# Performance work log

Measured on AMD Instinct MI355X. Metric: run time of the kernel, lower is better.

The kernel has to match this reference:

```python
import jax, jax.numpy as jnp
import numpy as np

NUM_EXPERTS = 8
TOP_K = 2
HIDDEN = 768
FFN = 3072
B, S = 4, 4096


def setup_inputs() -> dict:
    key = jax.random.key(0)
    ks = jax.random.split(key, 7)
    scale_h = 1.0 / np.sqrt(HIDDEN)
    scale_f = 1.0 / np.sqrt(FFN)
    return {
        "hidden_states": jax.random.normal(ks[0], (B, S, HIDDEN), dtype=jnp.float32),
        "router_w": jax.random.normal(ks[1], (HIDDEN, NUM_EXPERTS), dtype=jnp.float32) * scale_h,
        "router_b": jnp.zeros((NUM_EXPERTS,), dtype=jnp.float32),
        "w1": jax.random.normal(ks[2], (NUM_EXPERTS, HIDDEN, FFN), dtype=jnp.float32) * scale_h,
        "b1": jnp.zeros((NUM_EXPERTS, FFN), dtype=jnp.float32),
        "w2": jax.random.normal(ks[3], (NUM_EXPERTS, FFN, HIDDEN), dtype=jnp.float32) * scale_f,
        "b2": jnp.zeros((NUM_EXPERTS, HIDDEN), dtype=jnp.float32),
    }


def _moe_forward(x_flat, router_w, router_b, w1, b1, w2, b2):
    T = x_flat.shape[0]
    # Router: logits [T, E]
    router_logits = x_flat @ router_w + router_b
    routing_weights = jax.nn.softmax(router_logits, axis=-1)
    # Top-k gating: softmax over the selected top-k logits
    top_vals, top_idx = jax.lax.top_k(router_logits, TOP_K)
    top_gates = jax.nn.softmax(top_vals, axis=-1)
    # Scatter gates into dense dispatch mask [T, E]
    rows = jnp.arange(T)[:, None]
    dispatch_mask = jnp.zeros_like(routing_weights).at[rows, top_idx].set(top_gates)
    # Expert computation: combined = sum_e gate[:, e] * FFN_e(x)
    # (tokens with zero gate contribute exactly 0, matching the torch scatter-combine)
    combined = jnp.zeros_like(x_flat)
    for e in range(NUM_EXPERTS):
        h = jax.nn.gelu(x_flat @ w1[e] + b1[e])  # [T, FFN]
        y = h @ w2[e] + b2[e]                    # [T, HIDDEN]
        combined = combined + dispatch_mask[:, e:e + 1] * y
    # Auxiliary load-balancing loss
    mean_routing_prob = jnp.mean(routing_weights, axis=0)
    tokens_per_expert = jnp.sum(dispatch_mask, axis=0) / T
    aux_loss = jnp.sum(mean_routing_prob * tokens_per_expert) * NUM_EXPERTS
    return combined, routing_weights, dispatch_mask, aux_loss, router_logits


def reference(hidden_states, router_w, router_b, w1, b1, w2, b2):
    batch, seq, hid = hidden_states.shape
    x_flat = hidden_states.reshape(-1, hid)
    combined, routing_weights, dispatch_mask, aux_loss, router_logits = _moe_forward(
        x_flat, router_w, router_b, w1, b1, w2, b2)
    E = NUM_EXPERTS
    return (
        combined.reshape(batch, seq, hid),            # expert_outputs
        routing_weights.reshape(batch, seq, E),       # routing_weights
        dispatch_mask.reshape(batch, seq, E),         # dispatch_mask
        aux_loss,                                     # aux_loss
        router_logits.reshape(batch, seq, E),         # router_logits
    )
```

## Files before the change

kernel.cpp:

```cpp
#include <hip/hip_runtime.h>
#include <math.h>

#define TOKENS 16384
#define HID 768
#define FFN_DIM 3072
#define NEXP 8
#define MAXT 136

#define RT_TPB 128
#define RT_BLOCKS (TOKENS / RT_TPB)

typedef __bf16 bf16x8 __attribute__((ext_vector_type(8)));
typedef float f32x4 __attribute__((ext_vector_type(4)));

#define GLOBAL_AS(p) ((const __attribute__((address_space(1))) void*)(p))
#define LDS_AS(p)    ((__attribute__((address_space(3))) void*)(p))

__device__ __forceinline__ float gelu_f(float x) {
    const float x3 = x * x * x;
    const float z = 0.7978845608028654f * (x + 0.044715f * x3);
    const float e = __expf(2.f * z);
    const float t = 1.f - 2.f / (e + 1.f);
    return 0.5f * x * (1.f + t);
}

__device__ __forceinline__ unsigned short f2bf(float v) {
    return __builtin_bit_cast(unsigned short, (__bf16)v);
}

__global__ void __launch_bounds__(512) router_kernel(
    const float* __restrict__ x, const float* __restrict__ rw,
    const float* __restrict__ rb,
    float* __restrict__ out_rw, float* __restrict__ out_dm,
    float* __restrict__ out_logits,
    int* __restrict__ counts, float* __restrict__ probsum,
    float* __restrict__ gatesum, int* __restrict__ lists,
    float* __restrict__ glists)
{
    __shared__ int s_cnt[NEXP], s_base[NEXP];
    __shared__ float s_prob[NEXP], s_gate[NEXP];
    __shared__ int s_e1[RT_TPB], s_s1[RT_TPB], s_e2[RT_TPB], s_s2[RT_TPB];
    __shared__ float s_g1v[RT_TPB], s_g2v[RT_TPB];

    const int tid = threadIdx.x;
    if (tid < NEXP) { s_cnt[tid] = 0; s_prob[tid] = 0.f; s_gate[tid] = 0.f; }
    __syncthreads();

    const int wave = tid >> 6, lane = tid & 63;

    for (int it = 0; it < RT_TPB / 8; ++it) {
        const int lt = wave * (RT_TPB / 8) + it;
        const int t = blockIdx.x * RT_TPB + lt;
        const float* xr = x + (size_t)t * HID;
        float acc[NEXP];
#pragma unroll
        for (int e = 0; e < NEXP; ++e) acc[e] = 0.f;
#pragma unroll
        for (int j = 0; j < 12; ++j) {
            const int i = lane + (j << 6);
            const float xv = xr[i];
            const float4 a = ((const float4*)(rw + (size_t)i * NEXP))[0];
            const float4 b = ((const float4*)(rw + (size_t)i * NEXP))[1];
            acc[0] += xv * a.x; acc[1] += xv * a.y; acc[2] += xv * a.z; acc[3] += xv * a.w;
            acc[4] += xv * b.x; acc[5] += xv * b.y; acc[6] += xv * b.z; acc[7] += xv * b.w;
        }
#pragma unroll
        for (int off = 32; off > 0; off >>= 1)
#pragma unroll
            for (int e = 0; e < NEXP; ++e) acc[e] += __shfl_down(acc[e], off, 64);

        if (lane == 0) {
            float lg[NEXP];
            float m = -1e30f;
#pragma unroll
            for (int e = 0; e < NEXP; ++e) { lg[e] = acc[e] + rb[e]; m = fmaxf(m, lg[e]); }
            float ex[NEXP]; float s = 0.f;
#pragma unroll
            for (int e = 0; e < NEXP; ++e) { ex[e] = expf(lg[e] - m); s += ex[e]; }
            const float inv = 1.f / s;
            float* lrow = out_logits + (size_t)t * NEXP;
            float* prow = out_rw + (size_t)t * NEXP;
#pragma unroll
            for (int e = 0; e < NEXP; ++e) {
                lrow[e] = lg[e];
                const float p = ex[e] * inv;
                prow[e] = p;
                atomicAdd(&s_prob[e], p);
            }
            int i1 = 0;
#pragma unroll
            for (int e = 1; e < NEXP; ++e) if (lg[e] > lg[i1]) i1 = e;
            int i2 = (i1 == 0) ? 1 : 0;
#pragma unroll
            for (int e = 0; e < NEXP; ++e) if (e != i1 && lg[e] > lg[i2]) i2 = e;
            const float e2 = expf(lg[i2] - lg[i1]);
            const float g1 = 1.f / (1.f + e2);
            const float g2 = e2 / (1.f + e2);
            out_dm[(size_t)t * NEXP + i1] = g1;
            out_dm[(size_t)t * NEXP + i2] = g2;
            atomicAdd(&s_gate[i1], g1);
            atomicAdd(&s_gate[i2], g2);
            s_e1[lt] = i1; s_s1[lt] = atomicAdd(&s_cnt[i1], 1); s_g1v[lt] = g1;
            s_e2[lt] = i2; s_s2[lt] = atomicAdd(&s_cnt[i2], 1); s_g2v[lt] = g2;
        }
    }
    __syncthreads();
    if (tid < NEXP) {
        s_base[tid] = atomicAdd(&counts[tid], s_cnt[tid]);
        atomicAdd(&probsum[tid], s_prob[tid]);
        atomicAdd(&gatesum[tid], s_gate[tid]);
    }
    __syncthreads();
    if (tid < RT_TPB) {
        const int t = blockIdx.x * RT_TPB + tid;
        int e = s_e1[tid]; int p = s_base[e] + s_s1[tid];
        lists[e * TOKENS + p] = t; glists[e * TOKENS + p] = s_g1v[tid];
        e = s_e2[tid]; p = s_base[e] + s_s2[tid];
        lists[e * TOKENS + p] = t; glists[e * TOKENS + p] = s_g2v[tid];
    }
}

__global__ void finalize_kernel(const int* __restrict__ counts,
                                const float* __restrict__ probsum,
                                const float* __restrict__ gatesum,
                                int* __restrict__ poffs,
                                float* __restrict__ out_aux)
{
    if (threadIdx.x == 0 && blockIdx.x == 0) {
        float s = 0.f; int po = 0;
        for (int e = 0; e < NEXP; ++e) {
            poffs[e] = po;
            po += ((counts[e] + 255) >> 8) << 8;
            s += (probsum[e] / (float)TOKENS) * (gatesum[e] / (float)TOKENS);
        }
        poffs[NEXP] = po;
        *out_aux = s * (float)NEXP;
    }
}

__global__ void __launch_bounds__(192) gatherx_kernel(
    const float* __restrict__ x, const int* __restrict__ counts,
    const int* __restrict__ poffs, const int* __restrict__ lists,
    unsigned short* __restrict__ Xg)
{
    const int r = blockIdx.x;
    if (r >= poffs[NEXP]) return;
    int e = 0;
#pragma unroll
    for (int q = 1; q < NEXP; ++q) e += (r >= poffs[q]);
    const int ri = r - poffs[e];
    const int tid = threadIdx.x;
    uint2 o = make_uint2(0u, 0u);
    if (ri < counts[e]) {
        const int tok = lists[e * TOKENS + ri];
        const float4 v = *(const float4*)&x[(size_t)tok * HID + tid * 4];
        o.x = (unsigned)f2bf(v.x) | ((unsigned)f2bf(v.y) << 16);
        o.y = (unsigned)f2bf(v.z) | ((unsigned)f2bf(v.w) << 16);
    }
    *(uint2*)&Xg[(size_t)r * HID + tid * 4] = o;
}

__global__ void __launch_bounds__(256) convT_kernel(const float* __restrict__ in,
                                                    unsigned short* __restrict__ out,
                                                    int R, int C)
{
    __shared__ float sT[32][65];
    const int e = blockIdx.z;
    const float* in_e = in + (size_t)e * R * C;
    unsigned short* out_e = out + (size_t)e * R * C;
    const int r0 = blockIdx.y * 64;
    const int c0 = blockIdx.x * 32;
    const int tid = threadIdx.x;
    const int rr = tid >> 3, c4 = (tid & 7) * 4;
#pragma unroll
    for (int half = 0; half < 2; ++half) {
        const int r = rr + half * 32;
        const float4 v = *(const float4*)&in_e[(size_t)(r0 + r) * C + c0 + c4];
        sT[c4 + 0][r] = v.x; sT[c4 + 1][r] = v.y;
        sT[c4 + 2][r] = v.z; sT[c4 + 3][r] = v.w;
    }
    __syncthreads();
    const int c = tid >> 3, u = tid & 7;
    uint4 pk;
    const float* sr = &sT[c][u * 8];
    pk.x = (unsigned)f2bf(sr[0]) | ((unsigned)f2bf(sr[1]) << 16);
    pk.y = (unsigned)f2bf(sr[2]) | ((unsigned)f2bf(sr[3]) << 16);
    pk.z = (unsigned)f2bf(sr[4]) | ((unsigned)f2bf(sr[5]) << 16);
    pk.w = (unsigned)f2bf(sr[6]) | ((unsigned)f2bf(sr[7]) << 16);
    *(uint4*)&out_e[(size_t)(c0 + c) * R + r0 + u * 8] = pk;
}


#define STAGE1(bufE_, kt_) do { \
    _Pragma("unroll") \
    for (int _kh = 0; _kh < 2; ++_kh) { \
        const unsigned short* _pa = aStP + (kt_) * 64 + _kh * 32; \
        const unsigned short* _pb = bStP + (kt_) * 64 + _kh * 32; \
        __builtin_amdgcn_global_load_lds(GLOBAL_AS(_pa),           LDS_AS(aD + (bufE_) + _kh * 4096),       16, 0, 0); \
        __builtin_amdgcn_global_load_lds(GLOBAL_AS(_pa + 16 * KS), LDS_AS(aD + (bufE_) + _kh * 4096 + 512), 16, 0, 0); \
        __builtin_amdgcn_global_load_lds(GLOBAL_AS(_pb),           LDS_AS(bD + (bufE_) + _kh * 4096),       16, 0, 0); \
        __builtin_amdgcn_global_load_lds(GLOBAL_AS(_pb + 16 * KS), LDS_AS(bD + (bufE_) + _kh * 4096 + 512), 16, 0, 0); \
    } \
} while (0)

#define COMPUTE_TILE(curE_) do { \
    _Pragma("unroll") \
    for (int kh = 0; kh < 2; ++kh) { \
        bf16x8 af[4], bb[4]; \
        _Pragma("unroll") \
        for (int t = 0; t < 4; ++t) { \
            af[t] = *(const bf16x8*)&lds[(curE_) + kh * 4096 + (wm + t * 16 + fr) * 32 + swzR]; \
            bb[t] = *(const bf16x8*)&lds[16384 + (curE_) + kh * 4096 + (wn + t * 16 + fr) * 32 + swzR]; \
        } \
        _Pragma("unroll") \
        for (int tm = 0; tm < 4; ++tm) \
            _Pragma("unroll") \
            for (int tn = 0; tn < 4; ++tn) \
                acc[tm][tn] = __builtin_amdgcn_mfma_f32_16x16x32_bf16( \
                    af[tm], bb[tn], acc[tm][tn], 0, 0, 0); \
    } \
} while (0)

#define DECODE_TILE(NT_, MT_) \
    const int nwg = gridDim.x;                                                       \
    const int orig = blockIdx.x;                                                     \
    const int qq = nwg >> 3, rr2 = nwg & 7;                                          \
    const int xcd = orig & 7, pos = orig >> 3;                                       \
    const int wid = (xcd < rr2 ? xcd * (qq + 1) : rr2 * (qq + 1) + (xcd - rr2) * qq) + pos; \
    const int nSuper = (MT_) >> 3;                                                   \
    const int fullB = nSuper * 8 * (NT_);                                            \
    int mt, nti;                                                                     \
    if (wid < fullB) {                                                               \
        const int st_ = wid / (8 * (NT_));                                           \
        const int lo = wid - st_ * (8 * (NT_));                                      \
        mt = (st_ << 3) + (lo & 7);                                                  \
        nti = lo >> 3;                                                               \
    } else {                                                                         \
        const int rem = (MT_) - (nSuper << 3);                                       \
        const int lo = wid - fullB;                                                  \
        mt = (nSuper << 3) + lo % rem;                                               \
        nti = lo / rem;                                                              \
    }

__global__ void __launch_bounds__(256, 2) gemm1_kernel(
    const unsigned short* __restrict__ Xg, const unsigned short* __restrict__ W1T,
    const float* __restrict__ b1, const int* __restrict__ poffs,
    unsigned short* __restrict__ H, int grBase, int mtCount)
{
    extern __shared__ __bf16 lds[];
    const int KS = HID;
    const int NKT = HID / 64;

    DECODE_TILE(FFN_DIM / 128, mtCount)
    const int gr = grBase + mt * 128;
    if (gr >= poffs[NEXP]) return;
    int e = 0;
#pragma unroll
    for (int q = 1; q < NEXP; ++q) e += (gr >= poffs[q]);
    const int hbase = gr - grBase;
    const int n0 = nti * 128;

    const int tid = threadIdx.x;
    const int wv = tid >> 6, lane = tid & 63;
    const int wm = (wv >> 1) * 64, wn = (wv & 1) * 64;
    const int fr = lane & 15, q4 = lane >> 4;
    const int rowoff = lane >> 2;
    const int swzW = ((lane & 3) ^ ((lane >> 3) & 3)) << 3;
    const int swzR = (q4 ^ ((fr >> 1) & 3)) << 3;

    const unsigned short* aStP = Xg + (size_t)(gr + wv * 32 + rowoff) * KS + swzW;
    const unsigned short* bStP = W1T + (size_t)e * (HID * FFN_DIM)
                               + (size_t)(n0 + wv * 32 + rowoff) * KS + swzW;
    __bf16* aD = lds + wv * 1024;
    __bf16* bD = lds + 16384 + wv * 1024;

    f32x4 acc[4][4];
#pragma unroll
    for (int a = 0; a < 4; ++a)
#pragma unroll
        for (int b = 0; b < 4; ++b) acc[a][b] = (f32x4)(0.f);

    STAGE1(0, 0);
    __syncthreads();
#pragma unroll 2
    for (int kt = 0; kt < NKT; ++kt) {
        const int curE = (kt & 1) * 8192;
        if (kt + 1 < NKT) STAGE1(8192 - curE, kt + 1);
        COMPUTE_TILE(curE);
        __syncthreads();
    }

    const float* b1e = b1 + (size_t)e * FFN_DIM;
    float bias[4];
#pragma unroll
    for (int tn = 0; tn < 4; ++tn) bias[tn] = b1e[n0 + wn + tn * 16 + fr];
#pragma unroll
    for (int tm = 0; tm < 4; ++tm) {
#pragma unroll
        for (int tn = 0; tn < 4; ++tn) {
            const int n = n0 + wn + tn * 16 + fr;
#pragma unroll
            for (int r = 0; r < 4; ++r) {
                const int mloc = wm + tm * 16 + q4 * 4 + r;
                const float h = gelu_f(acc[tm][tn][r] + bias[tn]);
                H[(size_t)(hbase + mloc) * FFN_DIM + n] = f2bf(h);
            }
        }
    }
}

__global__ void __launch_bounds__(256, 2) gemm2_kernel(
    const unsigned short* __restrict__ H, const unsigned short* __restrict__ W2T,
    const float* __restrict__ b2, const int* __restrict__ counts,
    const int* __restrict__ poffs, const int* __restrict__ lists,
    const float* __restrict__ glists, float* __restrict__ out,
    int grBase, int mtCount)
{
    extern __shared__ __bf16 lds[];
    const int KS = FFN_DIM;
    const int NKT = FFN_DIM / 64;

    DECODE_TILE(HID / 128, mtCount)
    const int gr = grBase + mt * 128;
    if (gr >= poffs[NEXP]) return;
    int e = 0;
#pragma unroll
    for (int q = 1; q < NEXP; ++q) e += (gr >= poffs[q]);
    const int cnt = counts[e];
    const int m0 = gr - poffs[e];
    const int hbase = gr - grBase;
    const int n0 = nti * 128;

    int* sTok = (int*)&lds[32768];
    float* sGate = (float*)&lds[33024];

    const int tid = threadIdx.x;
    const int wv = tid >> 6, lane = tid & 63;
    const int wm = (wv >> 1) * 64, wn = (wv & 1) * 64;
    const int fr = lane & 15, q4 = lane >> 4;
    const int rowoff = lane >> 2;
    const int swzW = ((lane & 3) ^ ((lane >> 3) & 3)) << 3;
    const int swzR = (q4 ^ ((fr >> 1) & 3)) << 3;

    if (tid < 128) {
        int ri = m0 + tid; if (ri > cnt - 1) ri = cnt - 1;
        sTok[tid] = lists[e * TOKENS + ri];
        sGate[tid] = glists[e * TOKENS + ri];
    }

    const unsigned short* aStP = H + (size_t)(hbase + wv * 32 + rowoff) * KS + swzW;
    const unsigned short* bStP = W2T + (size_t)e * (HID * FFN_DIM)
                               + (size_t)(n0 + wv * 32 + rowoff) * KS + swzW;
    __bf16* aD = lds + wv * 1024;
    __bf16* bD = lds + 16384 + wv * 1024;

    f32x4 acc[4][4];
#pragma unroll
    for (int a = 0; a < 4; ++a)
#pragma unroll
        for (int b = 0; b < 4; ++b) acc[a][b] = (f32x4)(0.f);

    STAGE1(0, 0);
    __syncthreads();
#pragma unroll 2
    for (int kt = 0; kt < NKT; ++kt) {
        const int curE = (kt & 1) * 8192;
        if (kt + 1 < NKT) STAGE1(8192 - curE, kt + 1);
        COMPUTE_TILE(curE);
        __syncthreads();
    }

    const float* b2e = b2 + (size_t)e * HID;
    float bias[4];
#pragma unroll
    for (int tn = 0; tn < 4; ++tn) bias[tn] = b2e[n0 + wn + tn * 16 + fr];
#pragma unroll
    for (int tm = 0; tm < 4; ++tm) {
#pragma unroll
        for (int tn = 0; tn < 4; ++tn) {
            const int n = n0 + wn + tn * 16 + fr;
#pragma unroll
            for (int r = 0; r < 4; ++r) {
                const int mloc = wm + tm * 16 + q4 * 4 + r;
                if (m0 + mloc < cnt) {
                    const float y = acc[tm][tn][r] + bias[tn];
                    atomicAdd(&out[(size_t)sTok[mloc] * HID + n], sGate[mloc] * y);
                }
            }
        }
    }
}

#define BM 16
#define KC 64
#define XS 772
#define HS 68
__global__ void __launch_bounds__(256) ffn_kernel(
    const float* __restrict__ x, const float* __restrict__ w1,
    const float* __restrict__ b1, const float* __restrict__ w2,
    const float* __restrict__ b2, const int* __restrict__ counts,
    const int* __restrict__ lists, const float* __restrict__ glists,
    float* __restrict__ out)
{
    const int e = blockIdx.y;
    const int count = counts[e];
    const int row0 = blockIdx.x * BM;
    if (row0 >= count) return;

    __shared__ float sX[BM * XS];
    __shared__ float sH[BM * HS];
    __shared__ int sTokF[BM];
    __shared__ float sGateF[BM];
    const int tid = threadIdx.x;

    if (tid < BM) {
        const int ri = row0 + tid;
        int tok = 0; float g = 0.f;
        if (ri < count) { tok = lists[e * TOKENS + ri]; g = glists[e * TOKENS + ri]; }
        sTokF[tid] = tok; sGateF[tid] = g;
    }
    __syncthreads();
    {
        const int r = tid >> 4, q = tid & 15;
        const float4* src = (const float4*)(x + (size_t)sTokF[r] * HID);
#pragma unroll
        for (int j = 0; j < 12; ++j) {
            const float4 v = src[q + (j << 4)];
            *(float4*)&sX[r * XS + ((q + (j << 4)) << 2)] = v;
        }
    }
    __syncthreads();

    const float* w1e = w1 + (size_t)e * HID * FFN_DIM;
    const float* w2e = w2 + (size_t)e * FFN_DIM * HID;
    const float* b1e = b1 + (size_t)e * FFN_DIM;
    const float* b2e = b2 + (size_t)e * HID;
    const int r1 = tid & 15;
    const int c0 = (tid >> 4) << 2;
    const int c2 = (tid >> 4) * 48;

    float Y[48];
#pragma unroll
    for (int j = 0; j < 48; ++j) Y[j] = 0.f;

    for (int ch = 0; ch < FFN_DIM / KC; ++ch) {
        float h0 = 0.f, h1 = 0.f, h2 = 0.f, h3 = 0.f;
        const float* w1c = w1e + ch * KC + c0;
        for (int i = 0; i < HID; i += 4) {
            const float4 xv = *(const float4*)&sX[r1 * XS + i];
            const float* wp = w1c + (size_t)i * FFN_DIM;
            const float4 wa = *(const float4*)(wp);
            const float4 wb = *(const float4*)(wp + FFN_DIM);
            const float4 wc = *(const float4*)(wp + 2 * FFN_DIM);
            const float4 wd = *(const float4*)(wp + 3 * FFN_DIM);
            h0 += xv.x * wa.x + xv.y * wb.x + xv.z * wc.x + xv.w * wd.x;
            h1 += xv.x * wa.y + xv.y * wb.y + xv.z * wc.y + xv.w * wd.y;
            h2 += xv.x * wa.z + xv.y * wb.z + xv.z * wc.z + xv.w * wd.z;
            h3 += xv.x * wa.w + xv.y * wb.w + xv.z * wc.w + xv.w * wd.w;
        }
        const int cb = ch * KC + c0;
        h0 = gelu_f(h0 + b1e[cb + 0]);
        h1 = gelu_f(h1 + b1e[cb + 1]);
        h2 = gelu_f(h2 + b1e[cb + 2]);
        h3 = gelu_f(h3 + b1e[cb + 3]);
        __syncthreads();
        *(float4*)&sH[r1 * HS + c0] = make_float4(h0, h1, h2, h3);
        __syncthreads();
        const float* w2c = w2e + (size_t)ch * KC * HID + c2;
        for (int k = 0; k < KC; ++k) {
            const float hv = sH[r1 * HS + k];
            const float4* wr = (const float4*)(w2c + (size_t)k * HID);
#pragma unroll
            for (int j4 = 0; j4 < 12; ++j4) {
                const float4 wv = wr[j4];
                Y[j4 * 4 + 0] += hv * wv.x;
                Y[j4 * 4 + 1] += hv * wv.y;
                Y[j4 * 4 + 2] += hv * wv.z;
                Y[j4 * 4 + 3] += hv * wv.w;
            }
        }
    }
    const int ri = row0 + r1;
    if (ri < count) {
        const float g = sGateF[r1];
        float* orow = out + (size_t)sTokF[r1] * HID + c2;
#pragma unroll
        for (int j = 0; j < 48; ++j)
            atomicAdd(&orow[j], g * (Y[j] + b2e[c2 + j]));
    }
}

extern "C" void kernel_launch(void* const* d_in, const int* in_sizes, int n_in,
                              void* d_out, int out_size, void* d_ws, size_t ws_size,
                              hipStream_t stream)
{
    const float* x  = (const float*)d_in[0];
    const float* rw = (const float*)d_in[1];
    const float* rb = (const float*)d_in[2];
    const float* w1 = (const float*)d_in[3];
    const float* b1 = (const float*)d_in[4];
    const float* w2 = (const float*)d_in[5];
    const float* b2 = (const float*)d_in[6];

    float* out = (float*)d_out;
    float* out_comb   = out;
    float* out_rw     = out + (size_t)TOKENS * HID;
    float* out_dm     = out_rw + (size_t)TOKENS * NEXP;
    float* out_aux    = out_dm + (size_t)TOKENS * NEXP;
    float* out_logits = out_aux + 1;

    char* ws = (char*)d_ws;
    int*   counts  = (int*)ws;
    int*   poffs   = (int*)(ws + 64);
    float* probsum = (float*)(ws + 128);
    float* gatesum = (float*)(ws + 160);
    int*   lists   = (int*)(ws + 256);
    float* glists  = (float*)(ws + 256 + (size_t)NEXP * TOKENS * 4);
    size_t off = 256 + (size_t)NEXP * TOKENS * 8;
    off = (off + 255) & ~(size_t)255;
    unsigned short* Xg  = (unsigned short*)(ws + off); off += (size_t)MAXT * 256 * HID * 2;
    unsigned short* W1T = (unsigned short*)(ws + off); off += (size_t)NEXP * HID * FFN_DIM * 2;
    unsigned short* W2T = (unsigned short*)(ws + off); off += (size_t)NEXP * HID * FFN_DIM * 2;
    unsigned short* Hbuf = (unsigned short*)(ws + off);

    size_t avail = (ws_size > off) ? (ws_size - off) : 0;
    const int tilesFit = (int)(avail / ((size_t)256 * FFN_DIM * 2));
    int G = 0, tilesPG = 0;
    if (tilesFit >= 1) {
        G = (MAXT + tilesFit - 1) / tilesFit;
        tilesPG = (MAXT + G - 1) / G;
    }

    hipMemsetAsync(out_comb, 0, (size_t)TOKENS * HID * sizeof(float), stream);
    hipMemsetAsync(out_dm, 0, (size_t)TOKENS * NEXP * sizeof(float), stream);
    hipMemsetAsync(d_ws, 0, 256, stream);

    router_kernel<<<dim3(RT_BLOCKS), 512, 0, stream>>>(
        x, rw, rb, out_rw, out_dm, out_logits,
        counts, probsum, gatesum, lists, glists);
    finalize_kernel<<<1, 64, 0, stream>>>(counts, probsum, gatesum, poffs, out_aux);

    if (G > 0) {
        static int attr_done = 0;
        if (!attr_done) {
            hipFuncSetAttribute((const void*)gemm1_kernel,
                                hipFuncAttributeMaxDynamicSharedMemorySize, 65536);
            hipFuncSetAttribute((const void*)gemm2_kernel,
                                hipFuncAttributeMaxDynamicSharedMemorySize, 66560);
            attr_done = 1;
        }
        gatherx_kernel<<<dim3(MAXT * 256), 192, 0, stream>>>(
            x, counts, poffs, lists, Xg);
        convT_kernel<<<dim3(FFN_DIM / 32, HID / 64, NEXP), 256, 0, stream>>>(w1, W1T, HID, FFN_DIM);
        convT_kernel<<<dim3(HID / 32, FFN_DIM / 64, NEXP), 256, 0, stream>>>(w2, W2T, FFN_DIM, HID);
        for (int g = 0; g < G; ++g) {
            const int grBase = g * tilesPG * 256;
            const int mtCount = tilesPG * 2;
            gemm1_kernel<<<dim3(mtCount * (FFN_DIM / 128)), 256, 65536, stream>>>(
                Xg, W1T, b1, poffs, Hbuf, grBase, mtCount);
            gemm2_kernel<<<dim3(mtCount * (HID / 128)), 256, 66560, stream>>>(
                Hbuf, W2T, b2, counts, poffs, lists, glists, out_comb, grBase, mtCount);
        }
    } else {
        ffn_kernel<<<dim3(TOKENS / BM, NEXP), 256, 0, stream>>>(
            x, w1, b1, w2, b2, counts, lists, glists, out_comb);
    }
}
```

Before: 881.4 us.

## Enlarge expert GEMM tiles to 256-row blocks with 512-thread workgroups

Both grouped expert GEMMs now use 256-row M tiles and 8 waves per workgroup. GEMM1 moves to 256x256 tiles and GEMM2 to 256x128, with LDS buffers enlarged to match. The aim is more data reuse per LDS load and fewer global reads of weights and activations per FLOP. In exchange, each block uses more registers (GEMM1 holds 32 accumulators per wave) and 128KB of LDS, which may limit occupancy, and there are fewer blocks to fill the GPU.

New measurement: 886.0 us. No clear change (+0.5%).

```diff
diff --git a/kernel.cpp b/kernel.cpp
--- a/kernel.cpp
+++ b/kernel.cpp
@@ -191,34 +191,32 @@
 }
 
 
-#define STAGE1(bufE_, kt_) do { \
+#define STAGE_A256(bufE_, kt_) do { \
     _Pragma("unroll") \
-    for (int _kh = 0; _kh < 2; ++_kh) { \
-        const unsigned short* _pa = aStP + (kt_) * 64 + _kh * 32; \
-        const unsigned short* _pb = bStP + (kt_) * 64 + _kh * 32; \
-        __builtin_amdgcn_global_load_lds(GLOBAL_AS(_pa),           LDS_AS(aD + (bufE_) + _kh * 4096),       16, 0, 0); \
-        __builtin_amdgcn_global_load_lds(GLOBAL_AS(_pa + 16 * KS), LDS_AS(aD + (bufE_) + _kh * 4096 + 512), 16, 0, 0); \
-        __builtin_amdgcn_global_load_lds(GLOBAL_AS(_pb),           LDS_AS(bD + (bufE_) + _kh * 4096),       16, 0, 0); \
-        __builtin_amdgcn_global_load_lds(GLOBAL_AS(_pb + 16 * KS), LDS_AS(bD + (bufE_) + _kh * 4096 + 512), 16, 0, 0); \
-    } \
+    for (int _kh = 0; _kh < 2; ++_kh) \
+        _Pragma("unroll") \
+        for (int _rg = 0; _rg < 2; ++_rg) \
+            __builtin_amdgcn_global_load_lds( \
+                GLOBAL_AS(aStP + (kt_) * 64 + _kh * 32 + (size_t)_rg * 16 * KS), \
+                LDS_AS(lds + (bufE_) + _kh * 8192 + (wv * 32 + _rg * 16) * 32), 16, 0, 0); \
 } while (0)
 
-#define COMPUTE_TILE(curE_) do { \
+#define STAGE_B256(bufE_, kt_) do { \
     _Pragma("unroll") \
-    for (int kh = 0; kh < 2; ++kh) { \
-        bf16x8 af[4], bb[4]; \
+    for (int _kh = 0; _kh < 2; ++_kh) \
         _Pragma("unroll") \
-        for (int t = 0; t < 4; ++t) { \
-            af[t] = *(const bf16x8*)&lds[(curE_) + kh * 4096 + (wm + t * 16 + fr) * 32 + swzR]; \
-            bb[t] = *(const bf16x8*)&lds[16384 + (curE_) + kh * 4096 + (wn + t * 16 + fr) * 32 + swzR]; \
-        } \
-        _Pragma("unroll") \
-        for (int tm = 0; tm < 4; ++tm) \
-            _Pragma("unroll") \
-            for (int tn = 0; tn < 4; ++tn) \
-                acc[tm][tn] = __builtin_amdgcn_mfma_f32_16x16x32_bf16( \
-                    af[tm], bb[tn], acc[tm][tn], 0, 0, 0); \
-    } \
+        for (int _rg = 0; _rg < 2; ++_rg) \
+            __builtin_amdgcn_global_load_lds( \
+                GLOBAL_AS(bStP + (kt_) * 64 + _kh * 32 + (size_t)_rg * 16 * KS), \
+                LDS_AS(lds + (bufE_) + 16384 + _kh * 8192 + (wv * 32 + _rg * 16) * 32), 16, 0, 0); \
+} while (0)
+
+#define STAGE_B128(bufE_, kt_) do { \
+    _Pragma("unroll") \
+    for (int _kh = 0; _kh < 2; ++_kh) \
+        __builtin_amdgcn_global_load_lds( \
+            GLOBAL_AS(bStP + (kt_) * 64 + _kh * 32), \
+            LDS_AS(lds + (bufE_) + 16384 + _kh * 4096 + (wv * 16) * 32), 16, 0, 0); \
 } while (0)
 
 #define DECODE_TILE(NT_, MT_) \
@@ -242,7 +240,7 @@
         nti = lo / rem;                                                              \
     }
 
-__global__ void __launch_bounds__(256, 2) gemm1_kernel(
+__global__ void __launch_bounds__(512, 2) gemm1_kernel(
     const unsigned short* __restrict__ Xg, const unsigned short* __restrict__ W1T,
     const float* __restrict__ b1, const int* __restrict__ poffs,
     unsigned short* __restrict__ H, int grBase, int mtCount)
@@ -251,14 +249,99 @@
     const int KS = HID;
     const int NKT = HID / 64;
 
-    DECODE_TILE(FFN_DIM / 128, mtCount)
-    const int gr = grBase + mt * 128;
+    DECODE_TILE(FFN_DIM / 256, mtCount)
+    const int gr = grBase + mt * 256;
     if (gr >= poffs[NEXP]) return;
     int e = 0;
 #pragma unroll
     for (int q = 1; q < NEXP; ++q) e += (gr >= poffs[q]);
     const int hbase = gr - grBase;
+    const int n0 = nti * 256;
+
+    const int tid = threadIdx.x;
+    const int wv = tid >> 6, lane = tid & 63;
+    const int wm = (wv >> 2) * 128, wn = (wv & 3) * 64;
+    const int fr = lane & 15, q4 = lane >> 4;
+    const int rowoff = lane >> 2;
+    const int swzW = ((lane & 3) ^ ((lane >> 3) & 3)) << 3;
+    const int swzR = (q4 ^ ((fr >> 1) & 3)) << 3;
+
+    const unsigned short* aStP = Xg + (size_t)(gr + wv * 32 + rowoff) * KS + swzW;
+    const unsigned short* bStP = W1T + (size_t)e * (HID * FFN_DIM)
+                               + (size_t)(n0 + wv * 32 + rowoff) * KS + swzW;
+
+    f32x4 acc[8][4];
+#pragma unroll
+    for (int a = 0; a < 8; ++a)
+#pragma unroll
+        for (int b = 0; b < 4; ++b) acc[a][b] = (f32x4)(0.f);
+
+    STAGE_A256(0, 0); STAGE_B256(0, 0);
+    __syncthreads();
+#pragma unroll 2
+    for (int kt = 0; kt < NKT; ++kt) {
+        const int curE = (kt & 1) * 32768;
+        if (kt + 1 < NKT) { STAGE_A256(32768 - curE, kt + 1); STAGE_B256(32768 - curE, kt + 1); }
+#pragma unroll
+        for (int kh = 0; kh < 2; ++kh) {
+            bf16x8 af[8], bb[4];
+#pragma unroll
+            for (int mi = 0; mi < 8; ++mi)
+                af[mi] = *(const bf16x8*)&lds[curE + kh * 8192 + (wm + mi * 16 + fr) * 32 + swzR];
+#pragma unroll
+            for (int ni = 0; ni < 4; ++ni)
+                bb[ni] = *(const bf16x8*)&lds[curE + 16384 + kh * 8192 + (wn + ni * 16 + fr) * 32 + swzR];
+#pragma unroll
+            for (int mi = 0; mi < 8; ++mi)
+#pragma unroll
+                for (int ni = 0; ni < 4; ++ni)
+                    acc[mi][ni] = __builtin_amdgcn_mfma_f32_16x16x32_bf16(
+                        af[mi], bb[ni], acc[mi][ni], 0, 0, 0);
+        }
+        __syncthreads();
+    }
+
+    const float* b1e = b1 + (size_t)e * FFN_DIM;
+    float bias[4];
+#pragma unroll
+    for (int ni = 0; ni < 4; ++ni) bias[ni] = b1e[n0 + wn + ni * 16 + fr];
+#pragma unroll
+    for (int mi = 0; mi < 8; ++mi) {
+#pragma unroll
+        for (int r = 0; r < 4; ++r) {
+            const int m = wm + mi * 16 + q4 * 4 + r;
+            unsigned short* hp = H + (size_t)(hbase + m) * FFN_DIM + n0 + wn + fr;
+#pragma unroll
+            for (int ni = 0; ni < 4; ++ni)
+                hp[ni * 16] = f2bf(gelu_f(acc[mi][ni][r] + bias[ni]));
+        }
+    }
+}
+
+__global__ void __launch_bounds__(512, 2) gemm2_kernel(
+    const unsigned short* __restrict__ H, const unsigned short* __restrict__ W2T,
+    const float* __restrict__ b2, const int* __restrict__ counts,
+    const int* __restrict__ poffs, const int* __restrict__ lists,
+    const float* __restrict__ glists, float* __restrict__ out,
+    int grBase, int mtCount)
+{
+    extern __shared__ __bf16 lds[];
+    const int KS = FFN_DIM;
+    const int NKT = FFN_DIM / 64;
+
+    DECODE_TILE(HID / 128, mtCount)
+    const int gr = grBase + mt * 256;
+    if (gr >= poffs[NEXP]) return;
+    int e = 0;
+#pragma unroll
+    for (int q = 1; q < NEXP; ++q) e += (gr >= poffs[q]);
+    const int cnt = counts[e];
+    const int m0 = gr - poffs[e];
+    const int hbase = gr - grBase;
     const int n0 = nti * 128;
+
+    int* sTok = (int*)((char*)lds + 98304);
+    float* sGate = (float*)((char*)lds + 99328);
 
     const int tid = threadIdx.x;
     const int wv = tid >> 6, lane = tid & 63;
@@ -268,81 +351,7 @@
     const int swzW = ((lane & 3) ^ ((lane >> 3) & 3)) << 3;
     const int swzR = (q4 ^ ((fr >> 1) & 3)) << 3;
 
-    const unsigned short* aStP = Xg + (size_t)(gr + wv * 32 + rowoff) * KS + swzW;
-    const unsigned short* bStP = W1T + (size_t)e * (HID * FFN_DIM)
-                               + (size_t)(n0 + wv * 32 + rowoff) * KS + swzW;
-    __bf16* aD = lds + wv * 1024;
-    __bf16* bD = lds + 16384 + wv * 1024;
-
-    f32x4 acc[4][4];
-#pragma unroll
-    for (int a = 0; a < 4; ++a)
-#pragma unroll
-        for (int b = 0; b < 4; ++b) acc[a][b] = (f32x4)(0.f);
-
-    STAGE1(0, 0);
-    __syncthreads();
-#pragma unroll 2
-    for (int kt = 0; kt < NKT; ++kt) {
-        const int curE = (kt & 1) * 8192;
-        if (kt + 1 < NKT) STAGE1(8192 - curE, kt + 1);
-        COMPUTE_TILE(curE);
-        __syncthreads();
-    }
-
-    const float* b1e = b1 + (size_t)e * FFN_DIM;
-    float bias[4];
-#pragma unroll
-    for (int tn = 0; tn < 4; ++tn) bias[tn] = b1e[n0 + wn + tn * 16 + fr];
-#pragma unroll
-    for (int tm = 0; tm < 4; ++tm) {
-#pragma unroll
-        for (int tn = 0; tn < 4; ++tn) {
-            const int n = n0 + wn + tn * 16 + fr;
-#pragma unroll
-            for (int r = 0; r < 4; ++r) {
-                const int mloc = wm + tm * 16 + q4 * 4 + r;
-                const float h = gelu_f(acc[tm][tn][r] + bias[tn]);
-                H[(size_t)(hbase + mloc) * FFN_DIM + n] = f2bf(h);
-            }
-        }
-    }
-}
-
-__global__ void __launch_bounds__(256, 2) gemm2_kernel(
-    const unsigned short* __restrict__ H, const unsigned short* __restrict__ W2T,
-    const float* __restrict__ b2, const int* __restrict__ counts,
-    const int* __restrict__ poffs, const int* __restrict__ lists,
-    const float* __restrict__ glists, float* __restrict__ out,
-    int grBase, int mtCount)
-{
-    extern __shared__ __bf16 lds[];
-    const int KS = FFN_DIM;
-    const int NKT = FFN_DIM / 64;
-
-    DECODE_TILE(HID / 128, mtCount)
-    const int gr = grBase + mt * 128;
-    if (gr >= poffs[NEXP]) return;
-    int e = 0;
-#pragma unroll
-    for (int q = 1; q < NEXP; ++q) e += (gr >= poffs[q]);
-    const int cnt = counts[e];
-    const int m0 = gr - poffs[e];
-    const int hbase = gr - grBase;
-    const int n0 = nti * 128;
-
-    int* sTok = (int*)&lds[32768];
-    float* sGate = (float*)&lds[33024];
-
-    const int tid = threadIdx.x;
-    const int wv = tid >> 6, lane = tid & 63;
-    const int wm = (wv >> 1) * 64, wn = (wv & 1) * 64;
-    const int fr = lane & 15, q4 = lane >> 4;
-    const int rowoff = lane >> 2;
-    const int swzW = ((lane & 3) ^ ((lane >> 3) & 3)) << 3;
-    const int swzR = (q4 ^ ((fr >> 1) & 3)) << 3;
-
-    if (tid < 128) {
+    if (tid < 256) {
         int ri = m0 + tid; if (ri > cnt - 1) ri = cnt - 1;
         sTok[tid] = lists[e * TOKENS + ri];
         sGate[tid] = glists[e * TOKENS + ri];
@@ -350,9 +359,7 @@
 
     const unsigned short* aStP = H + (size_t)(hbase + wv * 32 + rowoff) * KS + swzW;
     const unsigned short* bStP = W2T + (size_t)e * (HID * FFN_DIM)
-                               + (size_t)(n0 + wv * 32 + rowoff) * KS + swzW;
-    __bf16* aD = lds + wv * 1024;
-    __bf16* bD = lds + 16384 + wv * 1024;
+                               + (size_t)(n0 + wv * 16 + rowoff) * KS + swzW;
 
     f32x4 acc[4][4];
 #pragma unroll
@@ -360,32 +367,47 @@
 #pragma unroll
         for (int b = 0; b < 4; ++b) acc[a][b] = (f32x4)(0.f);
 
-    STAGE1(0, 0);
+    STAGE_A256(0, 0); STAGE_B128(0, 0);
     __syncthreads();
 #pragma unroll 2
     for (int kt = 0; kt < NKT; ++kt) {
-        const int curE = (kt & 1) * 8192;
-        if (kt + 1 < NKT) STAGE1(8192 - curE, kt + 1);
-        COMPUTE_TILE(curE);
+        const int curE = (kt & 1) * 24576;
+        if (kt + 1 < NKT) { STAGE_A256(24576 - curE, kt + 1); STAGE_B128(24576 - curE, kt + 1); }
+#pragma unroll
+        for (int kh = 0; kh < 2; ++kh) {
+            bf16x8 af[4], bb[4];
+#pragma unroll
+            for (int mi = 0; mi < 4; ++mi)
+                af[mi] = *(const bf16x8*)&lds[curE + kh * 8192 + (wm + mi * 16 + fr) * 32 + swzR];
+#pragma unroll
+            for (int ni = 0; ni < 4; ++ni)
+                bb[ni] = *(const bf16x8*)&lds[curE + 16384 + kh * 4096 + (wn + ni * 16 + fr) * 32 + swzR];
+#pragma unroll
+            for (int mi = 0; mi < 4; ++mi)
+#pragma unroll
+                for (int ni = 0; ni < 4; ++ni)
+                    acc[mi][ni] = __builtin_amdgcn_mfma_f32_16x16x32_bf16(
+                        af[mi], bb[ni], acc[mi][ni], 0, 0, 0);
+        }
         __syncthreads();
     }
 
     const float* b2e = b2 + (size_t)e * HID;
     float bias[4];
 #pragma unroll
-    for (int tn = 0; tn < 4; ++tn) bias[tn] = b2e[n0 + wn + tn * 16 + fr];
-#pragma unroll
-    for (int tm = 0; tm < 4; ++tm) {
-#pragma unroll
-        for (int tn = 0; tn < 4; ++tn) {
-            const int n = n0 + wn + tn * 16 + fr;
-#pragma unroll
-            for (int r = 0; r < 4; ++r) {
-                const int mloc = wm + tm * 16 + q4 * 4 + r;
-                if (m0 + mloc < cnt) {
-                    const float y = acc[tm][tn][r] + bias[tn];
-                    atomicAdd(&out[(size_t)sTok[mloc] * HID + n], sGate[mloc] * y);
-                }
+    for (int ni = 0; ni < 4; ++ni) bias[ni] = b2e[n0 + wn + ni * 16 + fr];
+#pragma unroll
+    for (int mi = 0; mi < 4; ++mi) {
+#pragma unroll
+        for (int r = 0; r < 4; ++r) {
+            const int m = wm + mi * 16 + q4 * 4 + r;
+            if (m0 + m < cnt) {
+                const int tok = sTok[m];
+                const float g = sGate[m];
+                float* orow = out + (size_t)tok * HID + n0 + wn + fr;
+#pragma unroll
+                for (int ni = 0; ni < 4; ++ni)
+                    atomicAdd(&orow[ni * 16], g * (acc[mi][ni][r] + bias[ni]));
             }
         }
     }
@@ -544,9 +566,9 @@
         static int attr_done = 0;
         if (!attr_done) {
             hipFuncSetAttribute((const void*)gemm1_kernel,
-                                hipFuncAttributeMaxDynamicSharedMemorySize, 65536);
+                                hipFuncAttributeMaxDynamicSharedMemorySize, 131072);
             hipFuncSetAttribute((const void*)gemm2_kernel,
-                                hipFuncAttributeMaxDynamicSharedMemorySize, 66560);
+                                hipFuncAttributeMaxDynamicSharedMemorySize, 100352);
             attr_done = 1;
         }
         gatherx_kernel<<<dim3(MAXT * 256), 192, 0, stream>>>(
@@ -555,11 +577,10 @@
         convT_kernel<<<dim3(HID / 32, FFN_DIM / 64, NEXP), 256, 0, stream>>>(w2, W2T, FFN_DIM, HID);
         for (int g = 0; g < G; ++g) {
             const int grBase = g * tilesPG * 256;
-            const int mtCount = tilesPG * 2;
-            gemm1_kernel<<<dim3(mtCount * (FFN_DIM / 128)), 256, 65536, stream>>>(
-                Xg, W1T, b1, poffs, Hbuf, grBase, mtCount);
-            gemm2_kernel<<<dim3(mtCount * (HID / 128)), 256, 66560, stream>>>(
-                Hbuf, W2T, b2, counts, poffs, lists, glists, out_comb, grBase, mtCount);
+            gemm1_kernel<<<dim3(tilesPG * (FFN_DIM / 256)), 512, 131072, stream>>>(
+                Xg, W1T, b1, poffs, Hbuf, grBase, tilesPG);
+            gemm2_kernel<<<dim3(tilesPG * (HID / 128)), 512, 100352, stream>>>(
+                Hbuf, W2T, b2, counts, poffs, lists, glists, out_comb, grBase, tilesPG);
         }
     } else {
         ffn_kernel<<<dim3(TOKENS / BM, NEXP), 256, 0, stream>>>(
```
